# Optimization experiments

Hardware: AMD Instinct MI355X
Metric: run time of the kernel (lower is better)

The kernel has to match this reference:

```python
import jax, jax.numpy as jnp
import numpy as np

K = 3
K2 = K * K
EPS = 1e-5


def conv2d(x, w, b):
    # x: [B,C,H,W], w: [O,I,3,3] -> same-size conv, stride 1, pad 1
    y = jax.lax.conv_general_dilated(
        x, w, window_strides=(1, 1), padding=((1, 1), (1, 1)),
        dimension_numbers=("NCHW", "OIHW", "NCHW"))
    return y + b[None, :, None, None]


def setup_inputs() -> dict:
    key = jax.random.key(0)
    ks = jax.random.split(key, 9)
    B, Cin, Cout, H, W = 8, 64, 64, 128, 128
    inp = {
        "x": jax.random.normal(ks[0], (B, Cin, H, W), jnp.float32),
        # offset conv: small init so sampled offsets stay near the pixel grid
        "w_off": jax.random.normal(ks[1], (2 * K2, Cin, K, K), jnp.float32) * 0.01,
        "b_off": jnp.zeros((2 * K2,), jnp.float32),
        "w_mask": jax.random.normal(ks[2], (K2, Cin, K, K), jnp.float32) * 0.01,
        "b_mask": jnp.zeros((K2,), jnp.float32),
        "w_dcn": jax.random.normal(ks[3], (Cout, Cin, K, K), jnp.float32) * (1.0 / np.sqrt(Cin * K2)),
        "b_dcn": jnp.zeros((Cout,), jnp.float32),
        "gamma": jnp.ones((Cout,), jnp.float32),
        "beta": jnp.zeros((Cout,), jnp.float32),
    }
    return inp


def _deform_sample(img, py, px):
    # img: [C,H,W]; py,px: [K2,H,W] absolute sample coords (float)
    C, H, W = img.shape
    y0 = jnp.floor(py)
    x0 = jnp.floor(px)
    ly = py - y0  # frac weights [K2,H,W]
    lx = px - x0

    def gather(yi, xi):
        valid = (yi >= 0) & (yi < H) & (xi >= 0) & (xi < W)
        yc = jnp.clip(yi, 0, H - 1).astype(jnp.int32)
        xc = jnp.clip(xi, 0, W - 1).astype(jnp.int32)
        v = img[:, yc, xc]  # [C,K2,H,W]
        return v * valid[None].astype(img.dtype)

    v00 = gather(y0, x0)
    v01 = gather(y0, x0 + 1)
    v10 = gather(y0 + 1, x0)
    v11 = gather(y0 + 1, x0 + 1)
    w00 = ((1 - ly) * (1 - lx))[None]
    w01 = ((1 - ly) * lx)[None]
    w10 = (ly * (1 - lx))[None]
    w11 = (ly * lx)[None]
    return v00 * w00 + v01 * w01 + v10 * w10 + v11 * w11  # [C,K2,H,W]


def _dcn_forward(x, w_off, b_off, w_mask, b_mask, w_dcn, b_dcn, gamma, beta):
    B, Cin, H, W = x.shape
    Cout = w_dcn.shape[0]

    offset = conv2d(x, w_off, b_off)                    # [B,18,H,W]
    mask = jax.nn.sigmoid(conv2d(x, w_mask, b_mask))    # [B,9,H,W]

    off = offset.reshape(B, K2, 2, H, W)
    dy, dx = off[:, :, 0], off[:, :, 1]                 # [B,K2,H,W]

    ky = (jnp.arange(K2) // K - 1).astype(jnp.float32)  # kernel y offsets
    kx = (jnp.arange(K2) % K - 1).astype(jnp.float32)
    yy = jnp.arange(H, dtype=jnp.float32)
    xx = jnp.arange(W, dtype=jnp.float32)
    py = yy[None, None, :, None] + ky[None, :, None, None] + dy  # [B,K2,H,W]
    px = xx[None, None, None, :] + kx[None, :, None, None] + dx

    sampled = jax.vmap(_deform_sample)(x, py, px)       # [B,Cin,K2,H,W]
    cols = sampled * mask[:, None]                      # modulated columns

    out = jnp.einsum("bckhw,ock->bohw", cols, w_dcn.reshape(Cout, Cin, K2))
    out = out + b_dcn[None, :, None, None]

    # BatchNorm2d (training-mode batch statistics)
    mean = out.mean(axis=(0, 2, 3), keepdims=True)
    var = out.var(axis=(0, 2, 3), keepdims=True)
    out = (out - mean) * jax.lax.rsqrt(var + EPS)
    out = out * gamma[None, :, None, None] + beta[None, :, None, None]

    # Mish: x * tanh(softplus(x))
    return out * jnp.tanh(jnp.logaddexp(out, 0.0))


def reference(x, w_off, b_off, w_mask, b_mask, w_dcn, b_dcn, gamma, beta):
    return _dcn_forward(x, w_off, b_off, w_mask, b_mask, w_dcn, b_dcn, gamma, beta)
```

## Files before the change

kernel.cpp:

```cpp
#include <hip/hip_runtime.h>
#include <math.h>

#define BB 8
#define HH 128
#define WW 128
#define HW (HH*WW)
#define EPSV 1e-5f

typedef __attribute__((ext_vector_type(8))) _Float16 f16x8;
typedef __attribute__((ext_vector_type(4))) _Float16 f16x4;
typedef __attribute__((ext_vector_type(4))) float f32x4;

__device__ __forceinline__ short f2h(float f) {
    _Float16 h = (_Float16)f;
    return __builtin_bit_cast(short, h);
}
__device__ __forceinline__ f32x4 mfma_f16(f16x8 a, f16x8 b, f32x4 c) {
    return __builtin_amdgcn_mfma_f32_16x16x32_f16(a, b, c, 0, 0, 0);
}

__global__ __launch_bounds__(256) void prep_kernel(
    const float* __restrict__ x, short* __restrict__ xt,
    const float* __restrict__ w_dcn, const float* __restrict__ w_off,
    const float* __restrict__ w_mask,
    short* __restrict__ wtf_dcn, short* __restrict__ wtf_off)
{
    __shared__ short tl[4096];
    const int t = threadIdx.x;
    const int blk = blockIdx.x;

    if (blk < 216) {
        int i = blk * 256 + t;
        if (i < 36864) {
            int e = i & 7, lane = (i >> 3) & 63, nf = (i >> 9) & 3, ks = i >> 11;
            int tt = ks * 32 + ((lane >> 4) << 3) + e;
            int o = (nf << 4) + (lane & 15);
            int k = tt >> 6, c = tt & 63;
            wtf_dcn[i] = f2h(w_dcn[(o * 64 + c) * 9 + k]);
        } else {
            int j = i - 36864;
            int e = j & 7, lane = (j >> 3) & 63, nf = (j >> 9) & 1, ks = j >> 10;
            int tt = ks * 32 + ((lane >> 4) << 3) + e;
            int oc = (nf << 4) + (lane & 15);
            int k = tt >> 6, c = tt & 63;
            float v = 0.f;
            if (oc < 18) v = w_off[(oc * 64 + c) * 9 + k];
            else if (oc < 27) v = w_mask[((oc - 18) * 64 + c) * 9 + k];
            wtf_off[j] = f2h(v);
        }
    }

    const int b = blk >> 8, rem = blk & 255, h = rem >> 1, wb = (rem & 1) << 6;
    const int w4 = t & 15, ci = t >> 4;
#pragma unroll
    for (int i = 0; i < 4; ++i) {
        int c = i * 16 + ci;
        f32x4 v = *(const f32x4*)(x + (((b * 64 + c) * 128 + h) * 128) + wb + w4 * 4);
#pragma unroll
        for (int j = 0; j < 4; ++j) {
            int w = w4 * 4 + j;
            tl[w * 64 + (c ^ ((w & 7) << 3))] = f2h(v[j]);
        }
    }
    __syncthreads();
    const int p = t >> 2, q = t & 3;
    f16x8 a = *(const f16x8*)&tl[p * 64 + ((q * 16) ^ ((p & 7) << 3))];
    f16x8 bv = *(const f16x8*)&tl[p * 64 + ((q * 16 + 8) ^ ((p & 7) << 3))];
    short* dst = xt + ((((b << 7) | h) << 7) | (wb + p)) * 64 + q * 16;
    *(f16x8*)dst = a;
    *(f16x8*)(dst + 8) = bv;
}

__global__ __launch_bounds__(256, 4) void fused_conv(
    const short* __restrict__ xt,
    const short* __restrict__ wtf_off, const short* __restrict__ wtf_dcn,
    const float* __restrict__ b_off, const float* __restrict__ b_mask,
    const float* __restrict__ b_dcn,
    _Float16* __restrict__ preh, float* __restrict__ sums_p)
{
    __shared__ __align__(16) short alds[2][4096];
    __shared__ float offy[9][66], offxl[9][66], offmm[9][66];
    __shared__ float blkstats[2][64];

    const int tid = threadIdx.x;
    const int bid = blockIdx.x;
    if (tid < 128) blkstats[tid >> 6][tid & 63] = 0.f;

    const int tile = (bid & 7) * 256 + (bid >> 3);
    const int pbase = tile << 6;
    const int b = pbase / HW;
    const int rembase = pbase % HW;
    const int hh0 = rembase >> 7;
    const int wb0 = rembase & 127;
    const int p = tid >> 2, q = tid & 3;
    const int wp0 = wb0 + p;
    const int lane = tid & 63, wv = tid >> 6;
    const short* xb = xt + ((size_t)b << 20);

    const int ws0 = p * 64 + ((q * 16) ^ ((p & 7) << 3));
    const int ws1 = p * 64 + ((q * 16 + 8) ^ ((p & 7) << 3));

    const int nfw = wv & 1, mh = wv >> 1;
    f16x8 s0v, s1v;
    auto issueND = [&](int k) {
        int yy = hh0 + (k / 3) - 1;
        int xx = wp0 + (k % 3) - 1;
        bool ok = (yy >= 0) && (yy < HH) && (xx >= 0) && (xx < WW);
        const short* src = xb + (((((yy & 127) << 7) | (xx & 127))) << 6) + q * 16;
        f16x8 z = {};
        s0v = ok ? *(const f16x8*)src : z;
        s1v = ok ? *(const f16x8*)(src + 8) : z;
    };
    auto writeND = [&](int buf) {
        *(f16x8*)&alds[buf][ws0] = s0v;
        *(f16x8*)&alds[buf][ws1] = s1v;
    };

    f32x4 acc2[2];
    acc2[0] = (f32x4){0.f, 0.f, 0.f, 0.f};
    acc2[1] = acc2[0];

    issueND(0);
    writeND(0);
    __syncthreads();
    int s = 0;
#pragma unroll 1
    for (int k = 0; k < 9; ++k) {
        if (k < 8) issueND(k + 1);
        const short* bw = wtf_off + (4 * k + nfw) * 512;
        f16x8 b0 = *(const f16x8*)(bw + lane * 8);
        f16x8 b1 = *(const f16x8*)(bw + 1024 + lane * 8);
        __builtin_amdgcn_s_setprio(1);
#pragma unroll
        for (int kh = 0; kh < 2; ++kh) {
            f16x8 bb = kh ? b1 : b0;
#pragma unroll
            for (int i = 0; i < 2; ++i) {
                int px = (mh * 2 + i) * 16 + (lane & 15);
                int sidx = px * 64 + ((kh * 32 + ((lane >> 4) << 3)) ^ ((px & 7) << 3));
                f16x8 af = *(const f16x8*)&alds[s][sidx];
                acc2[i] = mfma_f16(af, bb, acc2[i]);
            }
        }
        __builtin_amdgcn_s_setprio(0);
        if (k < 8) writeND(s ^ 1);
        __syncthreads();
        s ^= 1;
    }
    {
        const int rq = lane >> 4;
        const int oc = nfw * 16 + (lane & 15);
#pragma unroll
        for (int i = 0; i < 2; ++i) {
#pragma unroll
            for (int j = 0; j < 4; ++j) {
                int px = (mh * 2 + i) * 16 + rq * 4 + j;
                float v = acc2[i][j];
                if (oc < 18) {
                    v += b_off[oc];
                    if (oc & 1) offxl[oc >> 1][px] = v; else offy[oc >> 1][px] = v;
                } else if (oc < 27) {
                    v += b_mask[oc - 18];
                    offmm[oc - 18][px] = 1.f / (1.f + __expf(-v));
                }
            }
        }
    }
    __syncthreads();

    const int nf = wv;
    f32x4 acc[4];
#pragma unroll
    for (int i = 0; i < 4; ++i) acc[i] = (f32x4){0.f, 0.f, 0.f, 0.f};

    f16x8 c00a, c00b, c01a, c01b, c10a, c10b, c11a, c11b;
    _Float16 h00, h01, h10, h11;
    auto bilin = [&](int k) {
        float dyv = offy[k][p], dxv = offxl[k][p], mv = offmm[k][p];
        float py  = (float)(hh0 + (k / 3) - 1) + dyv;
        float pxf = (float)(wp0 + (k % 3) - 1) + dxv;
        float y0f = floorf(py), x0f = floorf(pxf);
        float ly = py - y0f, lx = pxf - x0f;
        int y0 = (int)y0f, x0 = (int)x0f;
        int y1 = y0 + 1, x1 = x0 + 1;
        float fy0 = (y0 >= 0 && y0 < HH) ? 1.f : 0.f;
        float fy1 = (y1 >= 0 && y1 < HH) ? 1.f : 0.f;
        float fx0 = (x0 >= 0 && x0 < WW) ? 1.f : 0.f;
        float fx1 = (x1 >= 0 && x1 < WW) ? 1.f : 0.f;
        int yc0 = min(max(y0, 0), HH - 1), yc1 = min(max(y1, 0), HH - 1);
        int xc0 = min(max(x0, 0), WW - 1), xc1 = min(max(x1, 0), WW - 1);
        h00 = (_Float16)((1.f - ly) * (1.f - lx) * mv * fy0 * fx0);
        h01 = (_Float16)((1.f - ly) * lx * mv * fy0 * fx1);
        h10 = (_Float16)(ly * (1.f - lx) * mv * fy1 * fx0);
        h11 = (_Float16)(ly * lx * mv * fy1 * fx1);
        const short* s00 = xb + (((yc0 << 7) | xc0) << 6) + q * 16;
        const short* s01 = xb + (((yc0 << 7) | xc1) << 6) + q * 16;
        const short* s10 = xb + (((yc1 << 7) | xc0) << 6) + q * 16;
        const short* s11 = xb + (((yc1 << 7) | xc1) << 6) + q * 16;
        c00a = *(const f16x8*)s00; c00b = *(const f16x8*)(s00 + 8);
        c01a = *(const f16x8*)s01; c01b = *(const f16x8*)(s01 + 8);
        c10a = *(const f16x8*)s10; c10b = *(const f16x8*)(s10 + 8);
        c11a = *(const f16x8*)s11; c11b = *(const f16x8*)(s11 + 8);
    };
    auto writeB = [&](int buf) {
        f16x8 va = c00a * h00 + c01a * h01 + c10a * h10 + c11a * h11;
        f16x8 vb = c00b * h00 + c01b * h01 + c10b * h10 + c11b * h11;
        *(f16x8*)&alds[buf][ws0] = va;
        *(f16x8*)&alds[buf][ws1] = vb;
    };

    bilin(0);
    writeB(0);
    __syncthreads();
    s = 0;
#pragma unroll 1
    for (int k = 0; k < 9; ++k) {
        if (k < 8) bilin(k + 1);
        const short* bw = wtf_dcn + (((8 * k) + nf) * 64 + lane) * 8;
        f16x8 b0 = *(const f16x8*)bw;
        f16x8 b1 = *(const f16x8*)(bw + 2048);
        __builtin_amdgcn_s_setprio(1);
#pragma unroll
        for (int kh = 0; kh < 2; ++kh) {
            f16x8 bb = kh ? b1 : b0;
#pragma unroll
            for (int mb = 0; mb < 4; ++mb) {
                int px = mb * 16 + (lane & 15);
                int sidx = px * 64 + ((kh * 32 + ((lane >> 4) << 3)) ^ ((px & 7) << 3));
                f16x8 af = *(const f16x8*)&alds[s][sidx];
                acc[mb] = mfma_f16(af, bb, acc[mb]);
            }
        }
        __builtin_amdgcn_s_setprio(0);
        if (k < 8) writeB(s ^ 1);
        __syncthreads();
        s ^= 1;
    }

    {
        const int lr = lane & 15, rq = lane >> 4;
        const int o = nf * 16 + lr;
        const float bo = b_dcn[o];
        _Float16* dstp = preh + (size_t)(b * 64 + o) * HW + rembase;
        float sv = 0.f, s2 = 0.f;
#pragma unroll
        for (int mb = 0; mb < 4; ++mb) {
            f16x4 hv;
#pragma unroll
            for (int j = 0; j < 4; ++j) {
                float v = acc[mb][j] + bo;
                hv[j] = (_Float16)v;
                sv += v; s2 += v * v;
            }
            *(f16x4*)(dstp + mb * 16 + rq * 4) = hv;
        }
        sv += __shfl_xor(sv, 16);  sv += __shfl_xor(sv, 32);
        s2 += __shfl_xor(s2, 16);  s2 += __shfl_xor(s2, 32);
        if (lane < 16) {
            atomicAdd(&blkstats[0][o], sv);
            atomicAdd(&blkstats[1][o], s2);
        }
    }
    __syncthreads();
    if (tid < 64) {
        int slot = bid & 31;
        atomicAdd(&sums_p[tid * 32 + slot], blkstats[0][tid]);
        atomicAdd(&sums_p[2048 + tid * 32 + slot], blkstats[1][tid]);
    }
}

__global__ __launch_bounds__(256) void bn_mish(
    const _Float16* __restrict__ preh, const float* __restrict__ sums_p,
    const float* __restrict__ gamma, const float* __restrict__ beta,
    float* __restrict__ out)
{
    int vid = blockIdx.x * 256 + threadIdx.x;
    int c = (vid >> 11) & 63;
    const f32x4* sp = (const f32x4*)(sums_p + c * 32);
    const f32x4* sq4 = (const f32x4*)(sums_p + 2048 + c * 32);
    float sm = 0.f, sq = 0.f;
#pragma unroll
    for (int i = 0; i < 8; ++i) {
        f32x4 a = sp[i];  sm += a.x + a.y + a.z + a.w;
        f32x4 d = sq4[i]; sq += d.x + d.y + d.z + d.w;
    }
    const float invN = 1.f / (float)(BB * HW);
    float mean = sm * invN;
    float rstd = rsqrtf(sq * invN - mean * mean + EPSV);
    float g = gamma[c] * rstd;
    float be = beta[c] - mean * g;
    f16x8 v = ((const f16x8*)preh)[vid];
    float* dst = out + (size_t)vid * 8;
    f32x4 r0, r1;
#pragma unroll
    for (int j = 0; j < 8; ++j) {
        float t = (float)v[j] * g + be;
        float u = __expf(fminf(t, 20.f));
        float w = u * u + 2.f * u;
        float m = t * (w / (w + 2.f));
        if (j < 4) r0[j] = m; else r1[j - 4] = m;
    }
    *(f32x4*)dst = r0;
    *(f32x4*)(dst + 4) = r1;
}

extern "C" void kernel_launch(void* const* d_in, const int* in_sizes, int n_in,
                              void* d_out, int out_size, void* d_ws, size_t ws_size,
                              hipStream_t stream) {
    const float* x      = (const float*)d_in[0];
    const float* w_off  = (const float*)d_in[1];
    const float* b_off  = (const float*)d_in[2];
    const float* w_mask = (const float*)d_in[3];
    const float* b_mask = (const float*)d_in[4];
    const float* w_dcn  = (const float*)d_in[5];
    const float* b_dcn  = (const float*)d_in[6];
    const float* gamma  = (const float*)d_in[7];
    const float* beta   = (const float*)d_in[8];
    float* out = (float*)d_out;

    float* sums_p  = (float*)d_ws;
    short* wtf_dcn = (short*)(sums_p + 4096);
    short* wtf_off = wtf_dcn + 36864;
    short* xt      = wtf_off + 18432;
    _Float16* preh = (_Float16*)(xt + 8388608);

    hipMemsetAsync(sums_p, 0, 4096 * sizeof(float), stream);

    prep_kernel<<<2048, 256, 0, stream>>>(x, xt, w_dcn, w_off, w_mask, wtf_dcn, wtf_off);
    fused_conv<<<2048, 256, 0, stream>>>(xt, wtf_off, wtf_dcn, b_off, b_mask, b_dcn, preh, sums_p);
    bn_mish<<<4096, 256, 0, stream>>>(preh, sums_p, gamma, beta, out);
}
```

Before: 85.81 us.

## Deepen prefetch pipeline to two taps ahead in offset and deformable GEMM loops

Both main loops, the offset/mask conv and the deformable conv, become a two-stage register prefetch over kernel taps. Global gathers and weight fragment loads for tap k+2 and k+3 are issued before the current tap's MFMAs, and the loop is unrolled by two with ping-pong register sets. The intent is to hide global gather latency behind more MFMA work. In exchange, register pressure roughly doubles for the bilinear corner values, which could lower occupancy or cause spills.

Result: slower. 90.71 us (+5.7%).

```diff
diff --git a/kernel.cpp b/kernel.cpp
--- a/kernel.cpp
+++ b/kernel.cpp
@@ -101,51 +101,68 @@
     const int ws1 = p * 64 + ((q * 16 + 8) ^ ((p & 7) << 3));
 
     const int nfw = wv & 1, mh = wv >> 1;
-    f16x8 s0v, s1v;
-    auto issueND = [&](int k) {
+    auto issueND = [&](int k, f16x8& d0, f16x8& d1) {
         int yy = hh0 + (k / 3) - 1;
         int xx = wp0 + (k % 3) - 1;
         bool ok = (yy >= 0) && (yy < HH) && (xx >= 0) && (xx < WW);
         const short* src = xb + (((((yy & 127) << 7) | (xx & 127))) << 6) + q * 16;
         f16x8 z = {};
-        s0v = ok ? *(const f16x8*)src : z;
-        s1v = ok ? *(const f16x8*)(src + 8) : z;
-    };
-    auto writeND = [&](int buf) {
-        *(f16x8*)&alds[buf][ws0] = s0v;
-        *(f16x8*)&alds[buf][ws1] = s1v;
+        d0 = ok ? *(const f16x8*)src : z;
+        d1 = ok ? *(const f16x8*)(src + 8) : z;
+    };
+    auto writeND = [&](int buf, const f16x8& v0, const f16x8& v1) {
+        *(f16x8*)&alds[buf][ws0] = v0;
+        *(f16x8*)&alds[buf][ws1] = v1;
+    };
+    auto loadWA = [&](int k, f16x8& w0, f16x8& w1) {
+        const short* bw = wtf_off + (4 * k + nfw) * 512 + lane * 8;
+        w0 = *(const f16x8*)bw;
+        w1 = *(const f16x8*)(bw + 1024);
     };
 
     f32x4 acc2[2];
     acc2[0] = (f32x4){0.f, 0.f, 0.f, 0.f};
     acc2[1] = acc2[0];
 
-    issueND(0);
-    writeND(0);
-    __syncthreads();
-    int s = 0;
-#pragma unroll 1
-    for (int k = 0; k < 9; ++k) {
-        if (k < 8) issueND(k + 1);
-        const short* bw = wtf_off + (4 * k + nfw) * 512;
-        f16x8 b0 = *(const f16x8*)(bw + lane * 8);
-        f16x8 b1 = *(const f16x8*)(bw + 1024 + lane * 8);
+    auto mfmaA = [&](int buf, const f16x8& w0, const f16x8& w1) {
         __builtin_amdgcn_s_setprio(1);
 #pragma unroll
         for (int kh = 0; kh < 2; ++kh) {
-            f16x8 bb = kh ? b1 : b0;
+            f16x8 bb = kh ? w1 : w0;
 #pragma unroll
             for (int i = 0; i < 2; ++i) {
                 int px = (mh * 2 + i) * 16 + (lane & 15);
                 int sidx = px * 64 + ((kh * 32 + ((lane >> 4) << 3)) ^ ((px & 7) << 3));
-                f16x8 af = *(const f16x8*)&alds[s][sidx];
+                f16x8 af = *(const f16x8*)&alds[buf][sidx];
                 acc2[i] = mfma_f16(af, bb, acc2[i]);
             }
         }
         __builtin_amdgcn_s_setprio(0);
-        if (k < 8) writeND(s ^ 1);
+    };
+
+    {
+        f16x8 nA0, nA1, nB0, nB1, wa0, wa1, wbb0, wbb1;
+        issueND(0, nA0, nA1);
+        issueND(1, nB0, nB1);
+        loadWA(0, wa0, wa1);
+        loadWA(1, wbb0, wbb1);
+        writeND(0, nA0, nA1);
         __syncthreads();
-        s ^= 1;
+#pragma unroll 1
+        for (int k2 = 0; k2 < 4; ++k2) {
+            int k = k2 * 2;
+            if (k + 2 <= 8) issueND(k + 2, nA0, nA1);
+            mfmaA(0, wa0, wa1);
+            if (k + 2 <= 8) loadWA(k + 2, wa0, wa1);
+            writeND(1, nB0, nB1);
+            __syncthreads();
+            if (k + 3 <= 8) issueND(k + 3, nB0, nB1);
+            mfmaA(1, wbb0, wbb1);
+            if (k + 3 <= 8) loadWA(k + 3, wbb0, wbb1);
+            writeND(0, nA0, nA1);
+            __syncthreads();
+        }
+        mfmaA(0, wa0, wa1);
     }
     {
         const int rq = lane >> 4;
@@ -173,9 +190,8 @@
 #pragma unroll
     for (int i = 0; i < 4; ++i) acc[i] = (f32x4){0.f, 0.f, 0.f, 0.f};
 
-    f16x8 c00a, c00b, c01a, c01b, c10a, c10b, c11a, c11b;
-    _Float16 h00, h01, h10, h11;
-    auto bilin = [&](int k) {
+    auto bilinIssue = [&](int k, f16x8& d00a, f16x8& d00b, f16x8& d01a, f16x8& d01b,
+                          f16x8& d10a, f16x8& d10b, f16x8& d11a, f16x8& d11b, f16x4& hh) {
         float dyv = offy[k][p], dxv = offxl[k][p], mv = offmm[k][p];
         float py  = (float)(hh0 + (k / 3) - 1) + dyv;
         float pxf = (float)(wp0 + (k % 3) - 1) + dxv;
@@ -189,52 +205,76 @@
         float fx1 = (x1 >= 0 && x1 < WW) ? 1.f : 0.f;
         int yc0 = min(max(y0, 0), HH - 1), yc1 = min(max(y1, 0), HH - 1);
         int xc0 = min(max(x0, 0), WW - 1), xc1 = min(max(x1, 0), WW - 1);
-        h00 = (_Float16)((1.f - ly) * (1.f - lx) * mv * fy0 * fx0);
-        h01 = (_Float16)((1.f - ly) * lx * mv * fy0 * fx1);
-        h10 = (_Float16)(ly * (1.f - lx) * mv * fy1 * fx0);
-        h11 = (_Float16)(ly * lx * mv * fy1 * fx1);
+        hh[0] = (_Float16)((1.f - ly) * (1.f - lx) * mv * fy0 * fx0);
+        hh[1] = (_Float16)((1.f - ly) * lx * mv * fy0 * fx1);
+        hh[2] = (_Float16)(ly * (1.f - lx) * mv * fy1 * fx0);
+        hh[3] = (_Float16)(ly * lx * mv * fy1 * fx1);
         const short* s00 = xb + (((yc0 << 7) | xc0) << 6) + q * 16;
         const short* s01 = xb + (((yc0 << 7) | xc1) << 6) + q * 16;
         const short* s10 = xb + (((yc1 << 7) | xc0) << 6) + q * 16;
         const short* s11 = xb + (((yc1 << 7) | xc1) << 6) + q * 16;
-        c00a = *(const f16x8*)s00; c00b = *(const f16x8*)(s00 + 8);
-        c01a = *(const f16x8*)s01; c01b = *(const f16x8*)(s01 + 8);
-        c10a = *(const f16x8*)s10; c10b = *(const f16x8*)(s10 + 8);
-        c11a = *(const f16x8*)s11; c11b = *(const f16x8*)(s11 + 8);
-    };
-    auto writeB = [&](int buf) {
+        d00a = *(const f16x8*)s00; d00b = *(const f16x8*)(s00 + 8);
+        d01a = *(const f16x8*)s01; d01b = *(const f16x8*)(s01 + 8);
+        d10a = *(const f16x8*)s10; d10b = *(const f16x8*)(s10 + 8);
+        d11a = *(const f16x8*)s11; d11b = *(const f16x8*)(s11 + 8);
+    };
+    auto interpWrite = [&](int buf, const f16x8& c00a, const f16x8& c00b,
+                           const f16x8& c01a, const f16x8& c01b,
+                           const f16x8& c10a, const f16x8& c10b,
+                           const f16x8& c11a, const f16x8& c11b, const f16x4& hh) {
+        _Float16 h00 = hh[0], h01 = hh[1], h10 = hh[2], h11 = hh[3];
         f16x8 va = c00a * h00 + c01a * h01 + c10a * h10 + c11a * h11;
         f16x8 vb = c00b * h00 + c01b * h01 + c10b * h10 + c11b * h11;
         *(f16x8*)&alds[buf][ws0] = va;
         *(f16x8*)&alds[buf][ws1] = vb;
     };
-
-    bilin(0);
-    writeB(0);
-    __syncthreads();
-    s = 0;
-#pragma unroll 1
-    for (int k = 0; k < 9; ++k) {
-        if (k < 8) bilin(k + 1);
+    auto loadWB = [&](int k, f16x8& w0, f16x8& w1) {
         const short* bw = wtf_dcn + (((8 * k) + nf) * 64 + lane) * 8;
-        f16x8 b0 = *(const f16x8*)bw;
-        f16x8 b1 = *(const f16x8*)(bw + 2048);
+        w0 = *(const f16x8*)bw;
+        w1 = *(const f16x8*)(bw + 2048);
+    };
+    auto mfmaB = [&](int buf, const f16x8& w0, const f16x8& w1) {
         __builtin_amdgcn_s_setprio(1);
 #pragma unroll
         for (int kh = 0; kh < 2; ++kh) {
-            f16x8 bb = kh ? b1 : b0;
+            f16x8 bb = kh ? w1 : w0;
 #pragma unroll
             for (int mb = 0; mb < 4; ++mb) {
                 int px = mb * 16 + (lane & 15);
                 int sidx = px * 64 + ((kh * 32 + ((lane >> 4) << 3)) ^ ((px & 7) << 3));
-                f16x8 af = *(const f16x8*)&alds[s][sidx];
+                f16x8 af = *(const f16x8*)&alds[buf][sidx];
                 acc[mb] = mfma_f16(af, bb, acc[mb]);
             }
         }
         __builtin_amdgcn_s_setprio(0);
-        if (k < 8) writeB(s ^ 1);
+    };
+
+    {
+        f16x8 A00a, A00b, A01a, A01b, A10a, A10b, A11a, A11b;
+        f16x8 B00a, B00b, B01a, B01b, B10a, B10b, B11a, B11b;
+        f16x4 hA, hB;
+        f16x8 wa0, wa1, wbb0, wbb1;
+        bilinIssue(0, A00a, A00b, A01a, A01b, A10a, A10b, A11a, A11b, hA);
+        bilinIssue(1, B00a, B00b, B01a, B01b, B10a, B10b, B11a, B11b, hB);
+        loadWB(0, wa0, wa1);
+        loadWB(1, wbb0, wbb1);
+        interpWrite(0, A00a, A00b, A01a, A01b, A10a, A10b, A11a, A11b, hA);
         __syncthreads();
-        s ^= 1;
+#pragma unroll 1
+        for (int k2 = 0; k2 < 4; ++k2) {
+            int k = k2 * 2;
+            if (k + 2 <= 8) bilinIssue(k + 2, A00a, A00b, A01a, A01b, A10a, A10b, A11a, A11b, hA);
+            mfmaB(0, wa0, wa1);
+            if (k + 2 <= 8) loadWB(k + 2, wa0, wa1);
+            interpWrite(1, B00a, B00b, B01a, B01b, B10a, B10b, B11a, B11b, hB);
+            __syncthreads();
+            if (k + 3 <= 8) bilinIssue(k + 3, B00a, B00b, B01a, B01b, B10a, B10b, B11a, B11b, hB);
+            mfmaB(1, wbb0, wbb1);
+            if (k + 3 <= 8) loadWB(k + 3, wbb0, wbb1);
+            interpWrite(0, A00a, A00b, A01a, A01b, A10a, A10b, A11a, A11b, hA);
+            __syncthreads();
+        }
+        mfmaB(0, wa0, wa1);
     }
 
     {
```
